# Performance work log

Measured on AMD Instinct MI355X. Metric: run time of the kernel, lower is better.

Reference implementation:

```python
import jax, jax.numpy as jnp
import numpy as np

DIM = 1024
DEPTH = 8
DIM_HEAD = 64
HEADS = 16
NUM_Q = 16
EMB = 768
OUT = 1024
FF_INNER = 4 * DIM
INNER = DIM_HEAD * HEADS  # 1024
B, N1 = 64, 577
EPS = 1e-5


def _ln(x, g, b):
    mu = jnp.mean(x, axis=-1, keepdims=True)
    var = jnp.mean((x - mu) ** 2, axis=-1, keepdims=True)
    return (x - mu) * jax.lax.rsqrt(var + EPS) * g + b


def setup_inputs() -> dict:
    key = jax.random.key(0)
    ks = jax.random.split(key, 16)
    std = 0.02
    inp = {
        'x': jax.random.normal(ks[0], (B, N1, EMB), jnp.float32),
        'queries': jax.random.normal(ks[1], (1, NUM_Q, DIM), jnp.float32) / DIM ** 0.5,
        'proj_in_w': jax.random.normal(ks[2], (EMB, DIM), jnp.float32) * std,
        'proj_in_b': jnp.zeros((DIM,), jnp.float32),
        'ln1_g': jnp.ones((DEPTH, DIM), jnp.float32),
        'ln1_b': jnp.zeros((DEPTH, DIM), jnp.float32),
        'ln2_g': jnp.ones((DEPTH, DIM), jnp.float32),
        'ln2_b': jnp.zeros((DEPTH, DIM), jnp.float32),
        'wq': jax.random.normal(ks[3], (DEPTH, DIM, INNER), jnp.float32) * std,
        'wkv': jax.random.normal(ks[4], (DEPTH, DIM, 2 * INNER), jnp.float32) * std,
        'wo': jax.random.normal(ks[5], (DEPTH, INNER, DIM), jnp.float32) * std,
        'ffln_g': jnp.ones((DEPTH, DIM), jnp.float32),
        'ffln_b': jnp.zeros((DEPTH, DIM), jnp.float32),
        'w1': jax.random.normal(ks[6], (DEPTH, DIM, FF_INNER), jnp.float32) * std,
        'w2': jax.random.normal(ks[7], (DEPTH, FF_INNER, DIM), jnp.float32) * std,
        'proj_out_w': jax.random.normal(ks[8], (DIM, OUT), jnp.float32) * std,
        'proj_out_b': jnp.zeros((OUT,), jnp.float32),
        'nout_g': jnp.ones((OUT,), jnp.float32),
        'nout_b': jnp.zeros((OUT,), jnp.float32),
    }
    return inp


def reference(x, queries, proj_in_w, proj_in_b, ln1_g, ln1_b, ln2_g, ln2_b,
              wq, wkv, wo, ffln_g, ffln_b, w1, w2,
              proj_out_w, proj_out_b, nout_g, nout_b):
    b = x.shape[0]
    xp = x @ proj_in_w + proj_in_b          # (b, n1, dim)
    latents0 = jnp.broadcast_to(queries, (b, NUM_Q, DIM))
    scale = DIM_HEAD ** -0.25               # applied to both q and k

    def layer(latents, p):
        (g1, b1, g2, b2, Wq, Wkv, Wo, gf, bf, W1, W2) = p
        xn = _ln(xp, g1, b1)                # (b, n1, dim)
        lt = _ln(latents, g2, b2)           # (b, nq, dim)
        q = lt @ Wq                         # (b, nq, inner)
        kv_in = jnp.concatenate([xn, lt], axis=1)   # (b, n1+nq, dim)
        kv = kv_in @ Wkv                    # (b, n1+nq, 2*inner)
        k, v = jnp.split(kv, 2, axis=-1)
        L = kv_in.shape[1]
        qh = q.reshape(b, NUM_Q, HEADS, DIM_HEAD).transpose(0, 2, 1, 3)
        kh = k.reshape(b, L, HEADS, DIM_HEAD).transpose(0, 2, 1, 3)
        vh = v.reshape(b, L, HEADS, DIM_HEAD).transpose(0, 2, 1, 3)
        logits = jnp.einsum('bhqd,bhkd->bhqk', qh * scale, kh * scale)
        w = jax.nn.softmax(logits.astype(jnp.float32), axis=-1).astype(logits.dtype)
        o = jnp.einsum('bhqk,bhkd->bhqd', w, vh)
        o = o.transpose(0, 2, 1, 3).reshape(b, NUM_Q, INNER) @ Wo
        latents = o + latents
        h = _ln(latents, gf, bf) @ W1
        h = jax.nn.gelu(h, approximate=False)
        latents = h @ W2 + latents
        return latents, None

    params = (ln1_g, ln1_b, ln2_g, ln2_b, wq, wkv, wo, ffln_g, ffln_b, w1, w2)
    latents, _ = jax.lax.scan(layer, latents0, params)
    out = latents @ proj_out_w + proj_out_b
    return _ln(out, nout_g, nout_b)
```

## Files before the change

kernel.cpp:

```cpp
#include <hip/hip_runtime.h>
#include <hip/hip_bf16.h>
#include <math.h>

#define DEV __device__ __forceinline__

typedef __bf16 bf16x8 __attribute__((ext_vector_type(8)));
typedef float f32x4 __attribute__((ext_vector_type(4)));
typedef unsigned short u16x8 __attribute__((ext_vector_type(8)));
typedef unsigned short u16x4 __attribute__((ext_vector_type(4)));

DEV float b2f(unsigned short u){ unsigned int i = ((unsigned int)u)<<16; float f; __builtin_memcpy(&f,&i,4); return f; }
DEV unsigned short f2b(float x){ unsigned int i; __builtin_memcpy(&i,&x,4); unsigned int r = i + 0x7FFFu + ((i>>16)&1u); return (unsigned short)(r>>16); }

DEV int swz(int row, int elem){ return row*64 + ((((elem>>3) ^ row) & 7)<<3) + (elem&7); }

enum { EPI_F32=0, EPI_GELU=2, EPI_RESF32=3 };

constexpr int BKG = 64;

template<int BM, int BN, bool AF32>
__global__ __launch_bounds__(256)
void gemm_bt(const void* __restrict__ Ap, const unsigned short* __restrict__ Bt,
             const float* __restrict__ bias, unsigned short* __restrict__ Out,
             int M, int N, int K)
{
    constexpr int MR = BM/32, NR = BN/32;
    constexpr int LA = BM*BKG/(256*8);
    constexpr int LB = BN*BKG/(256*8);
    __shared__ unsigned short As[BM*64];
    __shared__ unsigned short Bs[BN*64];
    const int tid  = threadIdx.x;
    const int lane = tid & 63;
    const int wave = tid >> 6;
    const int wr = wave >> 1, wc = wave & 1;
    const int nt = blockIdx.x, mt = blockIdx.y;

    f32x4 acc[MR][NR];
    #pragma unroll
    for (int m=0;m<MR;m++)
      #pragma unroll
      for (int n=0;n<NR;n++) acc[m][n] = f32x4{0.f,0.f,0.f,0.f};

    u16x8 rA[LA]; f32x4 rAf[LA][2]; u16x8 rB[LB];

    auto issueA = [&](int k0){
      #pragma unroll
      for (int i=0;i<LA;i++){
        int e = (i*256+tid)*8; int row = e>>6, col = e&63;
        int gr = mt*BM + row; if (gr > M-1) gr = M-1;
        size_t ofs = (size_t)gr*K + (size_t)(k0+col);
        if constexpr (AF32){
          const f32x4* s = reinterpret_cast<const f32x4*>((const float*)Ap + ofs);
          rAf[i][0] = s[0]; rAf[i][1] = s[1];
        } else {
          rA[i] = *reinterpret_cast<const u16x8*>((const unsigned short*)Ap + ofs);
        }
      }
    };
    auto issueB = [&](int k0){
      #pragma unroll
      for (int i=0;i<LB;i++){
        int e = (i*256+tid)*8; int row = e>>6, col = e&63;
        size_t ofs = (size_t)(nt*BN+row)*K + (size_t)(k0+col);
        rB[i] = *reinterpret_cast<const u16x8*>(Bt + ofs);
      }
    };
    auto commit = [&](){
      #pragma unroll
      for (int i=0;i<LA;i++){
        int e = (i*256+tid)*8; int row = e>>6, col = e&63;
        u16x8 u;
        if constexpr (AF32){
          #pragma unroll
          for (int j=0;j<4;j++){ u[j] = f2b(rAf[i][0][j]); u[4+j] = f2b(rAf[i][1][j]); }
        } else u = rA[i];
        *reinterpret_cast<u16x8*>(&As[swz(row,col)]) = u;
      }
      #pragma unroll
      for (int i=0;i<LB;i++){
        int e = (i*256+tid)*8; int row = e>>6, col = e&63;
        *reinterpret_cast<u16x8*>(&Bs[swz(row,col)]) = rB[i];
      }
    };

    issueA(0); issueB(0);
    const int nk = K / BKG;
    #pragma unroll 1
    for (int kt=0; kt<nk; kt++){
      __syncthreads();
      commit();
      __syncthreads();
      if (kt+1 < nk){ issueA((kt+1)*BKG); issueB((kt+1)*BKG); }
      #pragma unroll
      for (int kk=0; kk<2; kk++){
        bf16x8 av[MR], bv[NR];
        #pragma unroll
        for (int m=0;m<MR;m++){
          int r = wr*(BM/2) + m*16 + (lane&15);
          av[m] = (bf16x8)(*reinterpret_cast<const u16x8*>(&As[swz(r, kk*32 + (lane>>4)*8)]));
        }
        #pragma unroll
        for (int n=0;n<NR;n++){
          int r = wc*(BN/2) + n*16 + (lane&15);
          bv[n] = (bf16x8)(*reinterpret_cast<const u16x8*>(&Bs[swz(r, kk*32 + (lane>>4)*8)]));
        }
        #pragma unroll
        for (int m=0;m<MR;m++)
          #pragma unroll
          for (int n=0;n<NR;n++)
            acc[m][n] = __builtin_amdgcn_mfma_f32_16x16x32_bf16(av[m], bv[n], acc[m][n], 0, 0, 0);
      }
    }

    #pragma unroll
    for (int m=0;m<MR;m++){
      #pragma unroll
      for (int n=0;n<NR;n++){
        #pragma unroll
        for (int r=0;r<4;r++){
          int row = mt*BM + wr*(BM/2) + m*16 + (lane>>4)*4 + r;
          int col = nt*BN + wc*(BN/2) + n*16 + (lane&15);
          if (row < M){
            float v = acc[m][n][r];
            if (bias) v += bias[col];
            Out[(size_t)row*N + col] = f2b(v);
          }
        }
      }
    }
}

template<int EPI>
__global__ __launch_bounds__(256)
void gemm_sp(const float* __restrict__ A,
             const unsigned short* __restrict__ BtH, const unsigned short* __restrict__ BtL,
             const float* __restrict__ bias, const float* __restrict__ Res,
             float* __restrict__ Out, int M, int N, int K)
{
    constexpr int BM=64, BN=64, MR=2, NR=2, LA=2, LB=2;
    __shared__ unsigned short As[2*BM*64];
    __shared__ unsigned short Bs[2*BN*64];
    const int tid  = threadIdx.x;
    const int lane = tid & 63;
    const int wave = tid >> 6;
    const int wr = wave >> 1, wc = wave & 1;
    const int mt = blockIdx.x, nt = blockIdx.y;

    f32x4 acc[MR][NR];
    #pragma unroll
    for (int m=0;m<MR;m++)
      #pragma unroll
      for (int n=0;n<NR;n++) acc[m][n] = f32x4{0.f,0.f,0.f,0.f};

    f32x4 rAf[LA][2]; u16x8 rBh[LB], rBl[LB];

    auto issueA = [&](int k0){
      #pragma unroll
      for (int i=0;i<LA;i++){
        int e = (i*256+tid)*8; int row = e>>6, col = e&63;
        const f32x4* s = reinterpret_cast<const f32x4*>(&A[(size_t)(mt*BM+row)*K + k0 + col]);
        rAf[i][0] = s[0]; rAf[i][1] = s[1];
      }
    };
    auto issueB = [&](int k0){
      #pragma unroll
      for (int i=0;i<LB;i++){
        int e = (i*256+tid)*8; int row = e>>6, col = e&63;
        size_t ofs = (size_t)(nt*BN+row)*K + (size_t)(k0+col);
        rBh[i] = *reinterpret_cast<const u16x8*>(BtH + ofs);
        rBl[i] = *reinterpret_cast<const u16x8*>(BtL + ofs);
      }
    };
    auto commit = [&](){
      #pragma unroll
      for (int i=0;i<LA;i++){
        int e = (i*256+tid)*8; int row = e>>6, col = e&63;
        u16x8 h, l;
        #pragma unroll
        for (int j=0;j<4;j++){
          float v0 = rAf[i][0][j], v1 = rAf[i][1][j];
          h[j]   = f2b(v0); l[j]   = f2b(v0 - b2f(h[j]));
          h[4+j] = f2b(v1); l[4+j] = f2b(v1 - b2f(h[4+j]));
        }
        int a = swz(row,col);
        *reinterpret_cast<u16x8*>(&As[a]) = h;
        *reinterpret_cast<u16x8*>(&As[BM*64 + a]) = l;
      }
      #pragma unroll
      for (int i=0;i<LB;i++){
        int e = (i*256+tid)*8; int row = e>>6, col = e&63;
        int a = swz(row,col);
        *reinterpret_cast<u16x8*>(&Bs[a]) = rBh[i];
        *reinterpret_cast<u16x8*>(&Bs[BN*64 + a]) = rBl[i];
      }
    };

    issueA(0); issueB(0);
    const int nk = K / BKG;
    #pragma unroll 1
    for (int kt=0; kt<nk; kt++){
      __syncthreads();
      commit();
      __syncthreads();
      if (kt+1 < nk){ issueA((kt+1)*BKG); issueB((kt+1)*BKG); }
      #pragma unroll
      for (int kk=0; kk<2; kk++){
        bf16x8 ah[MR], al[MR], bh[NR], bl[NR];
        #pragma unroll
        for (int m=0;m<MR;m++){
          int a = swz(wr*32 + m*16 + (lane&15), kk*32 + (lane>>4)*8);
          ah[m] = (bf16x8)(*reinterpret_cast<const u16x8*>(&As[a]));
          al[m] = (bf16x8)(*reinterpret_cast<const u16x8*>(&As[BM*64 + a]));
        }
        #pragma unroll
        for (int n=0;n<NR;n++){
          int a = swz(wc*32 + n*16 + (lane&15), kk*32 + (lane>>4)*8);
          bh[n] = (bf16x8)(*reinterpret_cast<const u16x8*>(&Bs[a]));
          bl[n] = (bf16x8)(*reinterpret_cast<const u16x8*>(&Bs[BN*64 + a]));
        }
        #pragma unroll
        for (int m=0;m<MR;m++)
          #pragma unroll
          for (int n=0;n<NR;n++){
            acc[m][n] = __builtin_amdgcn_mfma_f32_16x16x32_bf16(ah[m], bh[n], acc[m][n], 0, 0, 0);
            acc[m][n] = __builtin_amdgcn_mfma_f32_16x16x32_bf16(ah[m], bl[n], acc[m][n], 0, 0, 0);
            acc[m][n] = __builtin_amdgcn_mfma_f32_16x16x32_bf16(al[m], bh[n], acc[m][n], 0, 0, 0);
          }
      }
    }

    #pragma unroll
    for (int m=0;m<MR;m++){
      #pragma unroll
      for (int n=0;n<NR;n++){
        #pragma unroll
        for (int r=0;r<4;r++){
          int row = mt*BM + wr*32 + m*16 + (lane>>4)*4 + r;
          int col = nt*BN + wc*32 + n*16 + (lane&15);
          float v = acc[m][n][r];
          if (bias) v += bias[col];
          if constexpr (EPI==EPI_GELU)   v = 0.5f*v*(1.0f + erff(v*0.70710678118654752f));
          if constexpr (EPI==EPI_RESF32) v += Res[(size_t)row*N + col];
          Out[(size_t)row*N + col] = v;
        }
      }
    }
}

template<bool INF32, bool OUTF32, bool HASGB>
__global__ __launch_bounds__(256)
void ln_rows(const void* __restrict__ In, void* __restrict__ Out,
             const float* __restrict__ g, const float* __restrict__ bb)
{
  const int row = blockIdx.x;
  const int tid = threadIdx.x;
  const size_t base = (size_t)row*1024 + tid*4;
  float v[4];
  if constexpr (INF32){
    f32x4 t = *reinterpret_cast<const f32x4*>((const float*)In + base);
    v[0]=t[0]; v[1]=t[1]; v[2]=t[2]; v[3]=t[3];
  } else {
    u16x4 t = *reinterpret_cast<const u16x4*>((const unsigned short*)In + base);
    #pragma unroll
    for (int j=0;j<4;j++) v[j] = b2f(t[j]);
  }
  float s = v[0]+v[1]+v[2]+v[3];
  float q = v[0]*v[0]+v[1]*v[1]+v[2]*v[2]+v[3]*v[3];
  #pragma unroll
  for (int o=32;o>0;o>>=1){ s += __shfl_xor(s,o,64); q += __shfl_xor(q,o,64); }
  __shared__ float sm[8];
  const int wave = tid>>6, lane = tid&63;
  if (lane==0){ sm[wave] = s; sm[4+wave] = q; }
  __syncthreads();
  s = sm[0]+sm[1]+sm[2]+sm[3];
  q = sm[4]+sm[5]+sm[6]+sm[7];
  const float mean = s*(1.f/1024.f);
  const float rstd = rsqrtf(fmaxf(q*(1.f/1024.f) - mean*mean, 0.f) + 1e-5f);
  #pragma unroll
  for (int j=0;j<4;j++){
    float t2 = (v[j]-mean)*rstd;
    if constexpr (HASGB) t2 = t2*g[tid*4+j] + bb[tid*4+j];
    v[j] = t2;
  }
  if constexpr (OUTF32){
    f32x4 t{v[0],v[1],v[2],v[3]};
    *reinterpret_cast<f32x4*>((float*)Out + base) = t;
  } else {
    u16x4 t{f2b(v[0]),f2b(v[1]),f2b(v[2]),f2b(v[3])};
    *reinterpret_cast<u16x4*>((unsigned short*)Out + base) = t;
  }
}

template<bool LO>
__global__ __launch_bounds__(256)
void transpose_cvt(const float* __restrict__ W, const float* __restrict__ rs,
                   unsigned short* __restrict__ Wt, unsigned short* __restrict__ Wtlo,
                   int K, int N)
{
  __shared__ float t[32][33];
  const int tx = threadIdx.x & 31, ty = threadIdx.x >> 5;
  const int n0 = blockIdx.x*32, k0 = blockIdx.y*32;
  #pragma unroll
  for (int j=0;j<4;j++){
    int r = ty + j*8;
    float w = W[(size_t)(k0+r)*N + n0 + tx];
    if (rs) w *= rs[k0+r];
    t[r][tx] = w;
  }
  __syncthreads();
  #pragma unroll
  for (int j=0;j<4;j++){
    int r = ty + j*8;
    float w = t[tx][r];
    unsigned short hi = f2b(w);
    Wt[(size_t)(n0+r)*K + k0 + tx] = hi;
    if constexpr (LO)
      Wtlo[(size_t)(n0+r)*K + k0 + tx] = f2b(w - b2f(hi));
  }
}

__global__ __launch_bounds__(256)
void biaskv_kernel(const float* __restrict__ ln1b, const float* __restrict__ wkv,
                   float* __restrict__ out)
{
  const int l = blockIdx.y;
  const int n = blockIdx.x*256 + threadIdx.x;
  const float* b1 = ln1b + l*1024;
  const float* W  = wkv + (size_t)l*1024*2048;
  float s = 0.f;
  for (int k=0;k<1024;k++) s += b1[k]*W[(size_t)k*2048 + n];
  out[l*2048 + n] = s;
}

__global__ __launch_bounds__(256)
void init_latents(const float* __restrict__ Q, float* __restrict__ L)
{
  size_t idx = ((size_t)blockIdx.x*256 + threadIdx.x)*4;
  int row = (int)(idx >> 10);
  int col = (int)(idx & 1023);
  f32x4 t = *reinterpret_cast<const f32x4*>(Q + (size_t)(row & 15)*1024 + col);
  *reinterpret_cast<f32x4*>(L + idx) = t;
}

__global__ __launch_bounds__(256)
void attn_kernel(const float* __restrict__ QLTf,
                 const unsigned short* __restrict__ KVX,
                 const float* __restrict__ KVLTf,
                 float* __restrict__ ATTOf)
{
  __shared__ float qs[16][64];
  __shared__ float ws[16][600];
  const int tid = threadIdx.x;
  const int bh = blockIdx.x;
  const int b = bh >> 4, h = bh & 15;

  {
    int idx = tid*4;
    int qi = idx >> 6, d = idx & 63;
    f32x4 t = *reinterpret_cast<const f32x4*>(QLTf + (size_t)(b*16+qi)*1024 + h*64 + d);
    #pragma unroll
    for (int j=0;j<4;j++) qs[qi][d+j] = 0.125f * t[j];
  }
  __syncthreads();

  for (int r = tid; r < 593; r += 256){
    float a[16];
    #pragma unroll
    for (int qi=0;qi<16;qi++) a[qi] = 0.f;
    if (r < 577){
      const unsigned short* krow = KVX + ((size_t)(b*577 + r)*2048 + h*64);
      #pragma unroll 4
      for (int d4=0; d4<16; d4++){
        u16x4 k4 = *reinterpret_cast<const u16x4*>(krow + d4*4);
        float kf0=b2f(k4[0]), kf1=b2f(k4[1]), kf2=b2f(k4[2]), kf3=b2f(k4[3]);
        #pragma unroll
        for (int qi=0;qi<16;qi++){
          f32x4 q4 = *reinterpret_cast<const f32x4*>(&qs[qi][d4*4]);
          a[qi] += q4[0]*kf0 + q4[1]*kf1 + q4[2]*kf2 + q4[3]*kf3;
        }
      }
    } else {
      const float* krow = KVLTf + ((size_t)(b*16 + (r-577))*2048 + h*64);
      #pragma unroll 4
      for (int d4=0; d4<16; d4++){
        f32x4 k4 = *reinterpret_cast<const f32x4*>(krow + d4*4);
        #pragma unroll
        for (int qi=0;qi<16;qi++){
          f32x4 q4 = *reinterpret_cast<const f32x4*>(&qs[qi][d4*4]);
          a[qi] += q4[0]*k4[0] + q4[1]*k4[1] + q4[2]*k4[2] + q4[3]*k4[3];
        }
      }
    }
    #pragma unroll
    for (int qi=0;qi<16;qi++) ws[qi][r] = a[qi];
  }
  __syncthreads();

  const int wave = tid>>6, lane = tid&63;
  for (int qi = wave; qi < 16; qi += 4){
    float m = -1e30f;
    for (int r = lane; r < 593; r += 64) m = fmaxf(m, ws[qi][r]);
    #pragma unroll
    for (int o=32;o>0;o>>=1) m = fmaxf(m, __shfl_xor(m,o,64));
    float s = 0.f;
    for (int r = lane; r < 593; r += 64){ float e = expf(ws[qi][r]-m); ws[qi][r] = e; s += e; }
    #pragma unroll
    for (int o=32;o>0;o>>=1) s += __shfl_xor(s,o,64);
    float inv = 1.f/s;
    for (int r = lane; r < 593; r += 64) ws[qi][r] *= inv;
  }
  __syncthreads();

  const int d = tid & 63, qg = tid >> 6;
  float o0=0.f,o1=0.f,o2=0.f,o3=0.f;
  for (int rr=0; rr<576; rr+=4){
    f32x4 w0 = *reinterpret_cast<const f32x4*>(&ws[qg   ][rr]);
    f32x4 w1 = *reinterpret_cast<const f32x4*>(&ws[qg+4 ][rr]);
    f32x4 w2 = *reinterpret_cast<const f32x4*>(&ws[qg+8 ][rr]);
    f32x4 w3 = *reinterpret_cast<const f32x4*>(&ws[qg+12][rr]);
    #pragma unroll
    for (int j=0;j<4;j++){
      const unsigned short* vrow = KVX + ((size_t)(b*577 + rr + j)*2048 + 1024 + h*64);
      float v = b2f(vrow[d]);
      o0 += w0[j]*v; o1 += w1[j]*v; o2 += w2[j]*v; o3 += w3[j]*v;
    }
  }
  {
    float v = b2f(KVX[(size_t)(b*577 + 576)*2048 + 1024 + h*64 + d]);
    o0 += ws[qg][576]*v; o1 += ws[qg+4][576]*v; o2 += ws[qg+8][576]*v; o3 += ws[qg+12][576]*v;
  }
  for (int r=577; r<593; r++){
    float v = KVLTf[(size_t)(b*16 + (r-577))*2048 + 1024 + h*64 + d];
    o0 += ws[qg][r]*v; o1 += ws[qg+4][r]*v; o2 += ws[qg+8][r]*v; o3 += ws[qg+12][r]*v;
  }
  ATTOf[(size_t)(b*16+qg   )*1024 + h*64 + d] = o0;
  ATTOf[(size_t)(b*16+qg+4 )*1024 + h*64 + d] = o1;
  ATTOf[(size_t)(b*16+qg+8 )*1024 + h*64 + d] = o2;
  ATTOf[(size_t)(b*16+qg+12)*1024 + h*64 + d] = o3;
}

extern "C" void kernel_launch(void* const* d_in, const int* in_sizes, int n_in,
                              void* d_out, int out_size, void* d_ws, size_t ws_size,
                              hipStream_t stream)
{
  const float* x    = (const float*)d_in[0];
  const float* qry  = (const float*)d_in[1];
  const float* piw  = (const float*)d_in[2];
  const float* pib  = (const float*)d_in[3];
  const float* ln1g = (const float*)d_in[4];
  const float* ln1b = (const float*)d_in[5];
  const float* ln2g = (const float*)d_in[6];
  const float* ln2b = (const float*)d_in[7];
  const float* wq   = (const float*)d_in[8];
  const float* wkv  = (const float*)d_in[9];
  const float* wo   = (const float*)d_in[10];
  const float* ffg  = (const float*)d_in[11];
  const float* ffb  = (const float*)d_in[12];
  const float* w1   = (const float*)d_in[13];
  const float* w2   = (const float*)d_in[14];
  const float* pow_ = (const float*)d_in[15];
  const float* pob  = (const float*)d_in[16];
  const float* ng   = (const float*)d_in[17];
  const float* nb   = (const float*)d_in[18];

  const int MROWS = 64*577;
  char* wsb = (char*)d_ws;
  size_t off = 0;
  auto alloc = [&](size_t bytes)->char*{
    char* p = wsb + off; off = (off + bytes + 255) & ~(size_t)255; return p;
  };
  unsigned short* XP    = (unsigned short*)alloc((size_t)36992*1024*2);
  unsigned short* KVX   = (unsigned short*)alloc((size_t)36992*2048*2);
  unsigned short* WpiT  = (unsigned short*)alloc((size_t)1024*768*2);
  unsigned short* WkvTs = (unsigned short*)alloc((size_t)2048*1024*2);
  unsigned short* WkvT  = (unsigned short*)alloc((size_t)2048*1024*2);
  unsigned short* WkvTl = (unsigned short*)alloc((size_t)2048*1024*2);
  unsigned short* WqT   = (unsigned short*)alloc((size_t)1024*1024*2);
  unsigned short* WqTl  = (unsigned short*)alloc((size_t)1024*1024*2);
  unsigned short* WoT   = (unsigned short*)alloc((size_t)1024*1024*2);
  unsigned short* WoTl  = (unsigned short*)alloc((size_t)1024*1024*2);
  unsigned short* W1T   = (unsigned short*)alloc((size_t)4096*1024*2);
  unsigned short* W1Tl  = (unsigned short*)alloc((size_t)4096*1024*2);
  unsigned short* W2T   = (unsigned short*)alloc((size_t)1024*4096*2);
  unsigned short* W2Tl  = (unsigned short*)alloc((size_t)1024*4096*2);
  float*          BKV   = (float*)alloc((size_t)8*2048*4);
  float*          LTf   = (float*)alloc((size_t)1024*1024*4);
  float*          QLTf  = (float*)alloc((size_t)1024*1024*4);
  float*          KVLTf = (float*)alloc((size_t)1024*2048*4);
  float*          ATTOf = (float*)alloc((size_t)1024*1024*4);
  float*          FFHf  = (float*)alloc((size_t)1024*4096*4);
  float*          LATF  = (float*)alloc((size_t)1024*1024*4);
  if (off > ws_size) return;

  dim3 blk(256);

  transpose_cvt<false><<<dim3(32,24), blk, 0, stream>>>(piw, nullptr, WpiT, nullptr, 768, 1024);
  biaskv_kernel<<<dim3(8,8),   blk, 0, stream>>>(ln1b, wkv, BKV);
  init_latents<<<dim3(1024),   blk, 0, stream>>>(qry, LATF);

  gemm_bt<128,128,true><<<dim3(8,289), blk, 0, stream>>>(
      x, WpiT, pib, XP, MROWS, 1024, 768);
  ln_rows<false,false,false><<<dim3(MROWS), blk, 0, stream>>>(XP, XP, nullptr, nullptr);

  for (int l=0; l<8; l++){
    transpose_cvt<false><<<dim3(64,32),  blk, 0, stream>>>(wkv + (size_t)l*1024*2048, ln1g + l*1024, WkvTs, nullptr, 1024, 2048);
    transpose_cvt<true ><<<dim3(64,32),  blk, 0, stream>>>(wkv + (size_t)l*1024*2048, nullptr, WkvT, WkvTl, 1024, 2048);
    transpose_cvt<true ><<<dim3(32,32),  blk, 0, stream>>>(wq  + (size_t)l*1024*1024, nullptr, WqT,  WqTl, 1024, 1024);
    transpose_cvt<true ><<<dim3(32,32),  blk, 0, stream>>>(wo  + (size_t)l*1024*1024, nullptr, WoT,  WoTl, 1024, 1024);
    transpose_cvt<true ><<<dim3(128,32), blk, 0, stream>>>(w1  + (size_t)l*1024*4096, nullptr, W1T,  W1Tl, 1024, 4096);
    transpose_cvt<true ><<<dim3(32,128), blk, 0, stream>>>(w2  + (size_t)l*4096*1024, nullptr, W2T,  W2Tl, 4096, 1024);

    ln_rows<true,true,true><<<dim3(1024), blk, 0, stream>>>(LATF, LTf, ln2g + l*1024, ln2b + l*1024);
    gemm_sp<EPI_F32><<<dim3(16,16), blk, 0, stream>>>(
        LTf, WqT, WqTl, nullptr, nullptr, QLTf, 1024, 1024, 1024);
    gemm_sp<EPI_F32><<<dim3(16,32), blk, 0, stream>>>(
        LTf, WkvT, WkvTl, nullptr, nullptr, KVLTf, 1024, 2048, 1024);
    gemm_bt<128,128,false><<<dim3(16,289), blk, 0, stream>>>(
        XP, WkvTs, BKV + l*2048, KVX, MROWS, 2048, 1024);
    attn_kernel<<<dim3(1024), blk, 0, stream>>>(QLTf, KVX, KVLTf, ATTOf);
    gemm_sp<EPI_RESF32><<<dim3(16,16), blk, 0, stream>>>(
        ATTOf, WoT, WoTl, nullptr, LATF, LATF, 1024, 1024, 1024);
    ln_rows<true,true,true><<<dim3(1024), blk, 0, stream>>>(LATF, LTf, ffg + l*1024, ffb + l*1024);
    gemm_sp<EPI_GELU><<<dim3(16,64), blk, 0, stream>>>(
        LTf, W1T, W1Tl, nullptr, nullptr, FFHf, 1024, 4096, 1024);
    gemm_sp<EPI_RESF32><<<dim3(16,16), blk, 0, stream>>>(
        FFHf, W2T, W2Tl, nullptr, LATF, LATF, 1024, 1024, 4096);
  }

  transpose_cvt<true><<<dim3(32,32), blk, 0, stream>>>(pow_, nullptr, WqT, WqTl, 1024, 1024);
  gemm_sp<EPI_F32><<<dim3(16,16), blk, 0, stream>>>(
      LATF, WqT, WqTl, pob, nullptr, ATTOf, 1024, 1024, 1024);
  ln_rows<true,true,true><<<dim3(1024), blk, 0, stream>>>(ATTOf, d_out, ng, nb);
}
```

Baseline: 5.507 ms.

## Stage GEMM tiles with direct global-to-LDS loads and pre-split activations

The GEMM kernels now copy A and B tiles straight from global memory into swizzled LDS with global_load_lds, instead of staging them through registers. The split-precision GEMM now reads activations that upstream kernels (layernorm, attention, GELU epilogue) have already split into hi/lo bf16 pairs, so it no longer converts fp32 to bf16 inside its inner loop. The input x is converted to bf16 once up front, and blocks are remapped into 8 contiguous chunks to improve cache locality. In exchange, the register-prefetch double buffering is dropped: each k-step loads, syncs, computes and syncs again, so hiding memory latency now depends on occupancy.

```diff
diff --git a/kernel.cpp b/kernel.cpp
--- a/kernel.cpp
+++ b/kernel.cpp
@@ -16,24 +16,25 @@
 
 enum { EPI_F32=0, EPI_GELU=2, EPI_RESF32=3 };
 
-constexpr int BKG = 64;
-
-template<int BM, int BN, bool AF32>
-__global__ __launch_bounds__(256)
-void gemm_bt(const void* __restrict__ Ap, const unsigned short* __restrict__ Bt,
-             const float* __restrict__ bias, unsigned short* __restrict__ Out,
-             int M, int N, int K)
+template<int BM, int BN>
+__global__ __launch_bounds__(256)
+void gemm_lds(const unsigned short* __restrict__ A, const unsigned short* __restrict__ Bt,
+              const float* __restrict__ bias, unsigned short* __restrict__ Out,
+              int M, int N, int K, int NT)
 {
     constexpr int MR = BM/32, NR = BN/32;
-    constexpr int LA = BM*BKG/(256*8);
-    constexpr int LB = BN*BKG/(256*8);
+    constexpr int SA = BM/8, SB = BN/8;
     __shared__ unsigned short As[BM*64];
     __shared__ unsigned short Bs[BN*64];
     const int tid  = threadIdx.x;
     const int lane = tid & 63;
     const int wave = tid >> 6;
     const int wr = wave >> 1, wc = wave & 1;
-    const int nt = blockIdx.x, mt = blockIdx.y;
+    const int chunk = gridDim.x >> 3;
+    const int nb = (blockIdx.x & 7)*chunk + (blockIdx.x >> 3);
+    const int nt = nb % NT, mt = nb / NT;
+    const int lr = lane >> 3;
+    const int lc = lane & 7;
 
     f32x4 acc[MR][NR];
     #pragma unroll
@@ -41,56 +42,28 @@
       #pragma unroll
       for (int n=0;n<NR;n++) acc[m][n] = f32x4{0.f,0.f,0.f,0.f};
 
-    u16x8 rA[LA]; f32x4 rAf[LA][2]; u16x8 rB[LB];
-
-    auto issueA = [&](int k0){
-      #pragma unroll
-      for (int i=0;i<LA;i++){
-        int e = (i*256+tid)*8; int row = e>>6, col = e&63;
-        int gr = mt*BM + row; if (gr > M-1) gr = M-1;
-        size_t ofs = (size_t)gr*K + (size_t)(k0+col);
-        if constexpr (AF32){
-          const f32x4* s = reinterpret_cast<const f32x4*>((const float*)Ap + ofs);
-          rAf[i][0] = s[0]; rAf[i][1] = s[1];
-        } else {
-          rA[i] = *reinterpret_cast<const u16x8*>((const unsigned short*)Ap + ofs);
-        }
+    auto stage = [&](int k0){
+      #pragma unroll
+      for (int i=0;i<SA/4;i++){
+        int s = wave*(SA/4) + i;
+        int row = s*8 + lr;
+        const unsigned short* src = A + (size_t)(mt*BM+row)*K + k0 + (((lc ^ row)&7)<<3);
+        __builtin_amdgcn_global_load_lds((const unsigned int*)src, (unsigned int*)&As[s*512], 16, 0, 0);
+      }
+      #pragma unroll
+      for (int i=0;i<SB/4;i++){
+        int s = wave*(SB/4) + i;
+        int row = s*8 + lr;
+        const unsigned short* src = Bt + (size_t)(nt*BN+row)*K + k0 + (((lc ^ row)&7)<<3);
+        __builtin_amdgcn_global_load_lds((const unsigned int*)src, (unsigned int*)&Bs[s*512], 16, 0, 0);
       }
     };
-    auto issueB = [&](int k0){
-      #pragma unroll
-      for (int i=0;i<LB;i++){
-        int e = (i*256+tid)*8; int row = e>>6, col = e&63;
-        size_t ofs = (size_t)(nt*BN+row)*K + (size_t)(k0+col);
-        rB[i] = *reinterpret_cast<const u16x8*>(Bt + ofs);
-      }
-    };
-    auto commit = [&](){
-      #pragma unroll
-      for (int i=0;i<LA;i++){
-        int e = (i*256+tid)*8; int row = e>>6, col = e&63;
-        u16x8 u;
-        if constexpr (AF32){
-          #pragma unroll
-          for (int j=0;j<4;j++){ u[j] = f2b(rAf[i][0][j]); u[4+j] = f2b(rAf[i][1][j]); }
-        } else u = rA[i];
-        *reinterpret_cast<u16x8*>(&As[swz(row,col)]) = u;
-      }
-      #pragma unroll
-      for (int i=0;i<LB;i++){
-        int e = (i*256+tid)*8; int row = e>>6, col = e&63;
-        *reinterpret_cast<u16x8*>(&Bs[swz(row,col)]) = rB[i];
-      }
-    };
-
-    issueA(0); issueB(0);
-    const int nk = K / BKG;
+
+    const int nk = K / 64;
     #pragma unroll 1
     for (int kt=0; kt<nk; kt++){
+      stage(kt*64);
       __syncthreads();
-      commit();
-      __syncthreads();
-      if (kt+1 < nk){ issueA((kt+1)*BKG); issueB((kt+1)*BKG); }
       #pragma unroll
       for (int kk=0; kk<2; kk++){
         bf16x8 av[MR], bv[NR];
@@ -110,6 +83,7 @@
           for (int n=0;n<NR;n++)
             acc[m][n] = __builtin_amdgcn_mfma_f32_16x16x32_bf16(av[m], bv[n], acc[m][n], 0, 0, 0);
       }
+      __syncthreads();
     }
 
     #pragma unroll
@@ -132,19 +106,24 @@
 
 template<int EPI>
 __global__ __launch_bounds__(256)
-void gemm_sp(const float* __restrict__ A,
-             const unsigned short* __restrict__ BtH, const unsigned short* __restrict__ BtL,
+void gemm_sp(const unsigned short* __restrict__ AH, const unsigned short* __restrict__ AL,
+             const unsigned short* __restrict__ BH, const unsigned short* __restrict__ BL,
              const float* __restrict__ bias, const float* __restrict__ Res,
-             float* __restrict__ Out, int M, int N, int K)
-{
-    constexpr int BM=64, BN=64, MR=2, NR=2, LA=2, LB=2;
-    __shared__ unsigned short As[2*BM*64];
-    __shared__ unsigned short Bs[2*BN*64];
+             void* __restrict__ Out, unsigned short* __restrict__ OutL,
+             int M, int N, int K, int NT)
+{
+    constexpr int MR=2, NR=2;
+    __shared__ unsigned short As[2*64*64];
+    __shared__ unsigned short Bs[2*64*64];
     const int tid  = threadIdx.x;
     const int lane = tid & 63;
     const int wave = tid >> 6;
     const int wr = wave >> 1, wc = wave & 1;
-    const int mt = blockIdx.x, nt = blockIdx.y;
+    const int chunk = gridDim.x >> 3;
+    const int nb = (blockIdx.x & 7)*chunk + (blockIdx.x >> 3);
+    const int nt = nb % NT, mt = nb / NT;
+    const int lr = lane >> 3;
+    const int lc = lane & 7;
 
     f32x4 acc[MR][NR];
     #pragma unroll
@@ -152,57 +131,26 @@
       #pragma unroll
       for (int n=0;n<NR;n++) acc[m][n] = f32x4{0.f,0.f,0.f,0.f};
 
-    f32x4 rAf[LA][2]; u16x8 rBh[LB], rBl[LB];
-
-    auto issueA = [&](int k0){
-      #pragma unroll
-      for (int i=0;i<LA;i++){
-        int e = (i*256+tid)*8; int row = e>>6, col = e&63;
-        const f32x4* s = reinterpret_cast<const f32x4*>(&A[(size_t)(mt*BM+row)*K + k0 + col]);
-        rAf[i][0] = s[0]; rAf[i][1] = s[1];
+    auto stage = [&](int k0){
+      #pragma unroll
+      for (int i=0;i<2;i++){
+        int s = wave*2 + i;
+        int row = s*8 + lr;
+        int scol = ((lc ^ row)&7)<<3;
+        size_t aofs = (size_t)(mt*64+row)*K + k0 + scol;
+        size_t bofs = (size_t)(nt*64+row)*K + k0 + scol;
+        __builtin_amdgcn_global_load_lds((const unsigned int*)(AH+aofs), (unsigned int*)&As[s*512],        16, 0, 0);
+        __builtin_amdgcn_global_load_lds((const unsigned int*)(AL+aofs), (unsigned int*)&As[4096 + s*512], 16, 0, 0);
+        __builtin_amdgcn_global_load_lds((const unsigned int*)(BH+bofs), (unsigned int*)&Bs[s*512],        16, 0, 0);
+        __builtin_amdgcn_global_load_lds((const unsigned int*)(BL+bofs), (unsigned int*)&Bs[4096 + s*512], 16, 0, 0);
       }
     };
-    auto issueB = [&](int k0){
-      #pragma unroll
-      for (int i=0;i<LB;i++){
-        int e = (i*256+tid)*8; int row = e>>6, col = e&63;
-        size_t ofs = (size_t)(nt*BN+row)*K + (size_t)(k0+col);
-        rBh[i] = *reinterpret_cast<const u16x8*>(BtH + ofs);
-        rBl[i] = *reinterpret_cast<const u16x8*>(BtL + ofs);
-      }
-    };
-    auto commit = [&](){
-      #pragma unroll
-      for (int i=0;i<LA;i++){
-        int e = (i*256+tid)*8; int row = e>>6, col = e&63;
-        u16x8 h, l;
-        #pragma unroll
-        for (int j=0;j<4;j++){
-          float v0 = rAf[i][0][j], v1 = rAf[i][1][j];
-          h[j]   = f2b(v0); l[j]   = f2b(v0 - b2f(h[j]));
-          h[4+j] = f2b(v1); l[4+j] = f2b(v1 - b2f(h[4+j]));
-        }
-        int a = swz(row,col);
-        *reinterpret_cast<u16x8*>(&As[a]) = h;
-        *reinterpret_cast<u16x8*>(&As[BM*64 + a]) = l;
-      }
-      #pragma unroll
-      for (int i=0;i<LB;i++){
-        int e = (i*256+tid)*8; int row = e>>6, col = e&63;
-        int a = swz(row,col);
-        *reinterpret_cast<u16x8*>(&Bs[a]) = rBh[i];
-        *reinterpret_cast<u16x8*>(&Bs[BN*64 + a]) = rBl[i];
-      }
-    };
-
-    issueA(0); issueB(0);
-    const int nk = K / BKG;
+
+    const int nk = K / 64;
     #pragma unroll 1
     for (int kt=0; kt<nk; kt++){
+      stage(kt*64);
       __syncthreads();
-      commit();
-      __syncthreads();
-      if (kt+1 < nk){ issueA((kt+1)*BKG); issueB((kt+1)*BKG); }
       #pragma unroll
       for (int kk=0; kk<2; kk++){
         bf16x8 ah[MR], al[MR], bh[NR], bl[NR];
@@ -210,13 +158,13 @@
         for (int m=0;m<MR;m++){
           int a = swz(wr*32 + m*16 + (lane&15), kk*32 + (lane>>4)*8);
           ah[m] = (bf16x8)(*reinterpret_cast<const u16x8*>(&As[a]));
-          al[m] = (bf16x8)(*reinterpret_cast<const u16x8*>(&As[BM*64 + a]));
+          al[m] = (bf16x8)(*reinterpret_cast<const u16x8*>(&As[4096 + a]));
         }
         #pragma unroll
         for (int n=0;n<NR;n++){
           int a = swz(wc*32 + n*16 + (lane&15), kk*32 + (lane>>4)*8);
           bh[n] = (bf16x8)(*reinterpret_cast<const u16x8*>(&Bs[a]));
-          bl[n] = (bf16x8)(*reinterpret_cast<const u16x8*>(&Bs[BN*64 + a]));
+          bl[n] = (bf16x8)(*reinterpret_cast<const u16x8*>(&Bs[4096 + a]));
         }
         #pragma unroll
         for (int m=0;m<MR;m++)
@@ -227,6 +175,7 @@
             acc[m][n] = __builtin_amdgcn_mfma_f32_16x16x32_bf16(al[m], bh[n], acc[m][n], 0, 0, 0);
           }
       }
+      __syncthreads();
     }
 
     #pragma unroll
@@ -235,21 +184,29 @@
       for (int n=0;n<NR;n++){
         #pragma unroll
         for (int r=0;r<4;r++){
-          int row = mt*BM + wr*32 + m*16 + (lane>>4)*4 + r;
-          int col = nt*BN + wc*32 + n*16 + (lane&15);
+          int row = mt*64 + wr*32 + m*16 + (lane>>4)*4 + r;
+          int col = nt*64 + wc*32 + n*16 + (lane&15);
           float v = acc[m][n][r];
           if (bias) v += bias[col];
-          if constexpr (EPI==EPI_GELU)   v = 0.5f*v*(1.0f + erff(v*0.70710678118654752f));
-          if constexpr (EPI==EPI_RESF32) v += Res[(size_t)row*N + col];
-          Out[(size_t)row*N + col] = v;
+          if constexpr (EPI==EPI_GELU){
+            v = 0.5f*v*(1.0f + erff(v*0.70710678118654752f));
+            unsigned short hi = f2b(v);
+            ((unsigned short*)Out)[(size_t)row*N + col] = hi;
+            OutL[(size_t)row*N + col] = f2b(v - b2f(hi));
+          } else {
+            if constexpr (EPI==EPI_RESF32) v += Res[(size_t)row*N + col];
+            ((float*)Out)[(size_t)row*N + col] = v;
+          }
         }
       }
     }
 }
 
-template<bool INF32, bool OUTF32, bool HASGB>
+enum { OM_F32=0, OM_BF16=1, OM_SPLIT=2 };
+template<bool INF32, int OM, bool HASGB>
 __global__ __launch_bounds__(256)
 void ln_rows(const void* __restrict__ In, void* __restrict__ Out,
+             unsigned short* __restrict__ OutL,
              const float* __restrict__ g, const float* __restrict__ bb)
 {
   const int row = blockIdx.x;
@@ -282,12 +239,17 @@
     if constexpr (HASGB) t2 = t2*g[tid*4+j] + bb[tid*4+j];
     v[j] = t2;
   }
-  if constexpr (OUTF32){
+  if constexpr (OM==OM_F32){
     f32x4 t{v[0],v[1],v[2],v[3]};
     *reinterpret_cast<f32x4*>((float*)Out + base) = t;
-  } else {
+  } else if constexpr (OM==OM_BF16){
     u16x4 t{f2b(v[0]),f2b(v[1]),f2b(v[2]),f2b(v[3])};
     *reinterpret_cast<u16x4*>((unsigned short*)Out + base) = t;
+  } else {
+    u16x4 h{f2b(v[0]),f2b(v[1]),f2b(v[2]),f2b(v[3])};
+    u16x4 l{f2b(v[0]-b2f(h[0])),f2b(v[1]-b2f(h[1])),f2b(v[2]-b2f(h[2])),f2b(v[3]-b2f(h[3]))};
+    *reinterpret_cast<u16x4*>((unsigned short*)Out + base) = h;
+    *reinterpret_cast<u16x4*>(OutL + base) = l;
   }
 }
 
@@ -343,10 +305,33 @@
 }
 
 __global__ __launch_bounds__(256)
+void cvt_f32_bf16(const float* __restrict__ In, unsigned short* __restrict__ Out, size_t n4)
+{
+  size_t i = (size_t)blockIdx.x*256 + threadIdx.x;
+  if (i >= n4) return;
+  f32x4 t = *reinterpret_cast<const f32x4*>(In + i*4);
+  u16x4 u{f2b(t[0]),f2b(t[1]),f2b(t[2]),f2b(t[3])};
+  *reinterpret_cast<u16x4*>(Out + i*4) = u;
+}
+
+__global__ __launch_bounds__(256)
+void cvt_f32b_pair(const float* __restrict__ In, unsigned short* __restrict__ Oh,
+                   unsigned short* __restrict__ Ol)
+{
+  size_t idx = ((size_t)blockIdx.x*256 + threadIdx.x)*4;
+  f32x4 t = *reinterpret_cast<const f32x4*>(In + idx);
+  u16x4 h{f2b(t[0]),f2b(t[1]),f2b(t[2]),f2b(t[3])};
+  u16x4 l{f2b(t[0]-b2f(h[0])),f2b(t[1]-b2f(h[1])),f2b(t[2]-b2f(h[2])),f2b(t[3]-b2f(h[3]))};
+  *reinterpret_cast<u16x4*>(Oh + idx) = h;
+  *reinterpret_cast<u16x4*>(Ol + idx) = l;
+}
+
+__global__ __launch_bounds__(256)
 void attn_kernel(const float* __restrict__ QLTf,
                  const unsigned short* __restrict__ KVX,
                  const float* __restrict__ KVLTf,
-                 float* __restrict__ ATTOf)
+                 unsigned short* __restrict__ ATTOh,
+                 unsigned short* __restrict__ ATTOl)
 {
   __shared__ float qs[16][64];
   __shared__ float ws[16][600];
@@ -433,10 +418,14 @@
     float v = KVLTf[(size_t)(b*16 + (r-577))*2048 + 1024 + h*64 + d];
     o0 += ws[qg][r]*v; o1 += ws[qg+4][r]*v; o2 += ws[qg+8][r]*v; o3 += ws[qg+12][r]*v;
   }
-  ATTOf[(size_t)(b*16+qg   )*1024 + h*64 + d] = o0;
-  ATTOf[(size_t)(b*16+qg+4 )*1024 + h*64 + d] = o1;
-  ATTOf[(size_t)(b*16+qg+8 )*1024 + h*64 + d] = o2;
-  ATTOf[(size_t)(b*16+qg+12)*1024 + h*64 + d] = o3;
+  float ov[4] = {o0,o1,o2,o3};
+  #pragma unroll
+  for (int j=0;j<4;j++){
+    size_t idx = (size_t)(b*16+qg+4*j)*1024 + h*64 + d;
+    unsigned short hi = f2b(ov[j]);
+    ATTOh[idx] = hi;
+    ATTOl[idx] = f2b(ov[j] - b2f(hi));
+  }
 }
 
 extern "C" void kernel_launch(void* const* d_in, const int* in_sizes, int n_in,
@@ -469,6 +458,7 @@
   auto alloc = [&](size_t bytes)->char*{
     char* p = wsb + off; off = (off + bytes + 255) & ~(size_t)255; return p;
   };
+  unsigned short* XB    = (unsigned short*)alloc((size_t)36992*768*2);
   unsigned short* XP    = (unsigned short*)alloc((size_t)36992*1024*2);
   unsigned short* KVX   = (unsigned short*)alloc((size_t)36992*2048*2);
   unsigned short* WpiT  = (unsigned short*)alloc((size_t)1024*768*2);
@@ -484,23 +474,29 @@
   unsigned short* W2T   = (unsigned short*)alloc((size_t)1024*4096*2);
   unsigned short* W2Tl  = (unsigned short*)alloc((size_t)1024*4096*2);
   float*          BKV   = (float*)alloc((size_t)8*2048*4);
-  float*          LTf   = (float*)alloc((size_t)1024*1024*4);
+  unsigned short* LTh   = (unsigned short*)alloc((size_t)1024*1024*2);
+  unsigned short* LTl   = (unsigned short*)alloc((size_t)1024*1024*2);
   float*          QLTf  = (float*)alloc((size_t)1024*1024*4);
   float*          KVLTf = (float*)alloc((size_t)1024*2048*4);
-  float*          ATTOf = (float*)alloc((size_t)1024*1024*4);
-  float*          FFHf  = (float*)alloc((size_t)1024*4096*4);
+  unsigned short* ATTOh = (unsigned short*)alloc((size_t)1024*1024*2);
+  unsigned short* ATTOl = (unsigned short*)alloc((size_t)1024*1024*2);
+  unsigned short* FFHh  = (unsigned short*)alloc((size_t)1024*4096*2);
+  unsigned short* FFHl  = (unsigned short*)alloc((size_t)1024*4096*2);
+  unsigned short* LATBh = (unsigned short*)alloc((size_t)1024*1024*2);
+  unsigned short* LATBl = (unsigned short*)alloc((size_t)1024*1024*2);
   float*          LATF  = (float*)alloc((size_t)1024*1024*4);
   if (off > ws_size) return;
 
   dim3 blk(256);
 
+  cvt_f32_bf16<<<dim3((36928*768/4 + 255)/256), blk, 0, stream>>>(x, XB, (size_t)36928*768/4);
   transpose_cvt<false><<<dim3(32,24), blk, 0, stream>>>(piw, nullptr, WpiT, nullptr, 768, 1024);
   biaskv_kernel<<<dim3(8,8),   blk, 0, stream>>>(ln1b, wkv, BKV);
   init_latents<<<dim3(1024),   blk, 0, stream>>>(qry, LATF);
 
-  gemm_bt<128,128,true><<<dim3(8,289), blk, 0, stream>>>(
-      x, WpiT, pib, XP, MROWS, 1024, 768);
-  ln_rows<false,false,false><<<dim3(MROWS), blk, 0, stream>>>(XP, XP, nullptr, nullptr);
+  gemm_lds<128,128><<<dim3(8*289), blk, 0, stream>>>(
+      XB, WpiT, pib, XP, MROWS, 1024, 768, 8);
+  ln_rows<false,OM_BF16,false><<<dim3(MROWS), blk, 0, stream>>>(XP, XP, nullptr, nullptr, nullptr);
 
   for (int l=0; l<8; l++){
     transpose_cvt<false><<<dim3(64,32),  blk, 0, stream>>>(wkv + (size_t)l*1024*2048, ln1g + l*1024, WkvTs, nullptr, 1024, 2048);
@@ -510,25 +506,26 @@
     transpose_cvt<true ><<<dim3(128,32), blk, 0, stream>>>(w1  + (size_t)l*1024*4096, nullptr, W1T,  W1Tl, 1024, 4096);
     transpose_cvt<true ><<<dim3(32,128), blk, 0, stream>>>(w2  + (size_t)l*4096*1024, nullptr, W2T,  W2Tl, 4096, 1024);
 
-    ln_rows<true,true,true><<<dim3(1024), blk, 0, stream>>>(LATF, LTf, ln2g + l*1024, ln2b + l*1024);
-    gemm_sp<EPI_F32><<<dim3(16,16), blk, 0, stream>>>(
-        LTf, WqT, WqTl, nullptr, nullptr, QLTf, 1024, 1024, 1024);
-    gemm_sp<EPI_F32><<<dim3(16,32), blk, 0, stream>>>(
-        LTf, WkvT, WkvTl, nullptr, nullptr, KVLTf, 1024, 2048, 1024);
-    gemm_bt<128,128,false><<<dim3(16,289), blk, 0, stream>>>(
-        XP, WkvTs, BKV + l*2048, KVX, MROWS, 2048, 1024);
-    attn_kernel<<<dim3(1024), blk, 0, stream>>>(QLTf, KVX, KVLTf, ATTOf);
-    gemm_sp<EPI_RESF32><<<dim3(16,16), blk, 0, stream>>>(
-        ATTOf, WoT, WoTl, nullptr, LATF, LATF, 1024, 1024, 1024);
-    ln_rows<true,true,true><<<dim3(1024), blk, 0, stream>>>(LATF, LTf, ffg + l*1024, ffb + l*1024);
-    gemm_sp<EPI_GELU><<<dim3(16,64), blk, 0, stream>>>(
-        LTf, W1T, W1Tl, nullptr, nullptr, FFHf, 1024, 4096, 1024);
-    gemm_sp<EPI_RESF32><<<dim3(16,16), blk, 0, stream>>>(
-        FFHf, W2T, W2Tl, nullptr, LATF, LATF, 1024, 1024, 4096);
+    ln_rows<true,OM_SPLIT,true><<<dim3(1024), blk, 0, stream>>>(LATF, LTh, LTl, ln2g + l*1024, ln2b + l*1024);
+    gemm_sp<EPI_F32><<<dim3(16*16), blk, 0, stream>>>(
+        LTh, LTl, WqT, WqTl, nullptr, nullptr, QLTf, nullptr, 1024, 1024, 1024, 16);
+    gemm_sp<EPI_F32><<<dim3(16*32), blk, 0, stream>>>(
+        LTh, LTl, WkvT, WkvTl, nullptr, nullptr, KVLTf, nullptr, 1024, 2048, 1024, 32);
+    gemm_lds<128,128><<<dim3(16*289), blk, 0, stream>>>(
+        XP, WkvTs, BKV + l*2048, KVX, MROWS, 2048, 1024, 16);
+    attn_kernel<<<dim3(1024), blk, 0, stream>>>(QLTf, KVX, KVLTf, ATTOh, ATTOl);
+    gemm_sp<EPI_RESF32><<<dim3(16*16), blk, 0, stream>>>(
+        ATTOh, ATTOl, WoT, WoTl, nullptr, LATF, LATF, nullptr, 1024, 1024, 1024, 16);
+    ln_rows<true,OM_SPLIT,true><<<dim3(1024), blk, 0, stream>>>(LATF, LTh, LTl, ffg + l*1024, ffb + l*1024);
+    gemm_sp<EPI_GELU><<<dim3(16*64), blk, 0, stream>>>(
+        LTh, LTl, W1T, W1Tl, nullptr, nullptr, FFHh, FFHl, 1024, 4096, 1024, 64);
+    gemm_sp<EPI_RESF32><<<dim3(16*16), blk, 0, stream>>>(
+        FFHh, FFHl, W2T, W2Tl, nullptr, LATF, LATF, nullptr, 1024, 1024, 4096, 16);
   }
 
   transpose_cvt<true><<<dim3(32,32), blk, 0, stream>>>(pow_, nullptr, WqT, WqTl, 1024, 1024);
-  gemm_sp<EPI_F32><<<dim3(16,16), blk, 0, stream>>>(
-      LATF, WqT, WqTl, pob, nullptr, ATTOf, 1024, 1024, 1024);
-  ln_rows<true,true,true><<<dim3(1024), blk, 0, stream>>>(ATTOf, d_out, ng, nb);
-}
+  cvt_f32b_pair<<<dim3(1024), blk, 0, stream>>>(LATF, LATBh, LATBl);
+  gemm_sp<EPI_F32><<<dim3(16*16), blk, 0, stream>>>(
+      LATBh, LATBl, WqT, WqTl, pob, nullptr, QLTf, nullptr, 1024, 1024, 1024, 16);
+  ln_rows<true,OM_F32,true><<<dim3(1024), blk, 0, stream>>>(QLTf, d_out, nullptr, ng, nb);
+}
```

Measured after the change: 6.099 ms. 1.11x slower.
